# Performance work log

Hardware: AMD Instinct MI355X
Metric: run time of the kernel (lower is better)

The kernel has to match this reference:

```python
import jax, jax.numpy as jnp
import numpy as np

N = 50000       # nodes (src == dst set for both blocks)
E = 800000      # edges (avg degree 16)
IN_DIM = 64     # input node feature dim ('attr')
POT_DIM = 16    # potential feature dim ('pot')
H = 64          # h_dim == out_dim == out_edim


def setup_inputs() -> dict:
    key = jax.random.key(0)
    ks = jax.random.split(key, 14)
    g = lambda k, shape, scale: jax.random.normal(k, shape, dtype=jnp.float32) * scale
    return {
        'attr':    g(ks[0], (N, IN_DIM), 1.0),
        'pot0':    g(ks[1], (N, POT_DIM), 1.0),
        'pot1':    g(ks[2], (N, POT_DIM), 1.0),
        'edge_t0': g(ks[3], (E, H), 1.0),
        'edge_t1': g(ks[4], (E, H), 1.0),
        # pot_encoder: Linear(pot_dim, h_dim) + Tanh
        'Wpot': g(ks[5], (POT_DIM, H), POT_DIM ** -0.5),
        'bpot': jnp.zeros((H,), jnp.float32),
        # layer 0: GATLayer(in_dim, h, h, h)
        'fcW0': g(ks[6], (IN_DIM, H), IN_DIM ** -0.5),
        'fcU0': g(ks[7], (IN_DIM, H), IN_DIM ** -0.5),
        'a0':   g(ks[8], (3 * H,), (3 * H) ** -0.5),   # attn_fc weight [z_src|z_dst|t]
        'gate0': jnp.ones((H,), jnp.float32),
        # layer 1: GATLayer(h, h, h, h)
        'fcW1': g(ks[9], (H, H), H ** -0.5),
        'fcU1': g(ks[10], (H, H), H ** -0.5),
        'a1':   g(ks[11], (3 * H,), (3 * H) ** -0.5),
        'gate1': jnp.ones((H,), jnp.float32),
        'src_idx': jax.random.randint(ks[12], (E,), 0, N),
        'dst_idx': jax.random.randint(ks[13], (E,), 0, N),
    }


def _gat_layer(h, v_i, t, src, dst, fcW, fcU, a, gate):
    # h: [N, Din], v_i: [N, H], t: [E, H] (raw edge data 'd'->'t' per original forward)
    Hd = fcW.shape[1]
    z = h @ fcW                 # [N, H] srcdata['z']
    z_i = h @ fcU               # [N, H] dstdata['z_i'] (src set == dst set)
    a_src, a_dst, a_t = a[:Hd], a[Hd:2 * Hd], a[2 * Hd:]
    # attn_fc(cat[z_src, z_dst, t]) decomposed into per-node + per-edge dot products
    score = jax.nn.leaky_relu((z @ a_src)[src] + (z @ a_dst)[dst] + t @ a_t,
                              negative_slope=0.01)        # [E]
    # edge softmax over each dst node's incoming edges
    m = jax.ops.segment_max(score, dst, num_segments=N)   # [N]
    ex = jnp.exp(score - m[dst])                          # [E]
    denom = jax.ops.segment_sum(ex, dst, num_segments=N)  # [N]
    alpha = ex / jnp.where(denom == 0, 1.0, denom)[dst]   # [E]
    z_neighbor = jax.ops.segment_sum(alpha[:, None] * z[src], dst, num_segments=N)
    return z_neighbor + gate * v_i * z_i                  # [N, H]


def reference(attr, pot0, pot1, edge_t0, edge_t1, Wpot, bpot,
              fcW0, fcU0, a0, gate0, fcW1, fcU1, a1, gate1,
              src_idx, dst_idx):
    v0 = jnp.tanh(pot0 @ Wpot + bpot)
    h = _gat_layer(attr, v0, edge_t0, src_idx, dst_idx, fcW0, fcU0, a0, gate0)
    v1 = jnp.tanh(pot1 @ Wpot + bpot)
    h = _gat_layer(h, v1, edge_t1, src_idx, dst_idx, fcW1, fcU1, a1, gate1)
    return h
```

## Files before the change

### kernel.cpp

```cpp
#include <hip/hip_runtime.h>
#include <math.h>

#define NN 50000
#define EE 800000
#define BM 64
#define HB 3125
#define DB 1250
#define DS_ (DB * 256)
#define TB 782

typedef float f4 __attribute__((ext_vector_type(4)));


#define FMA4(acc, s, v) do { \
    (acc).x = fmaf((s), (v).x, (acc).x); \
    (acc).y = fmaf((s), (v).y, (acc).y); \
    (acc).z = fmaf((s), (v).z, (acc).z); \
    (acc).w = fmaf((s), (v).w, (acc).w); } while (0)

__device__ __forceinline__ float dot4(float4 u, float4 v) {
    return fmaf(u.x, v.x, fmaf(u.y, v.y, fmaf(u.z, v.z, u.w * v.w)));
}

__device__ __forceinline__ unsigned pk_bf16(float lo, float hi) {
    union { float f; unsigned u; } a, b;
    a.f = lo; b.f = hi;
    unsigned alo = (a.u + 0x7FFFu + ((a.u >> 16) & 1u)) >> 16;
    unsigned bhi = (b.u + 0x7FFFu + ((b.u >> 16) & 1u)) >> 16;
    return (bhi << 16) | alo;
}

__device__ __forceinline__ float upk_bf16(unsigned u, int odd) {
    union { unsigned u; float f; } r;
    r.u = odd ? (u & 0xFFFF0000u) : (u << 16);
    return r.f;
}


__global__ __launch_bounds__(256) void hist_dot(
    const int* __restrict__ dst, int* __restrict__ deg, int* __restrict__ rank,
    const float* __restrict__ et0, const float* __restrict__ et1,
    const float* __restrict__ a0, const float* __restrict__ a1,
    float* __restrict__ sc0, float* __restrict__ sc1)
{
    const int bid = blockIdx.x;

    if (bid < HB) {
        const int e = bid * 256 + threadIdx.x;
        rank[e] = atomicAdd(&deg[dst[e]], 1);
    } else {
        const int tid  = (bid - HB) * 256 + threadIdx.x;
        const int lane = threadIdx.x & 63;
        const int p    = tid & 15;
        const float4 A0 = *reinterpret_cast<const float4*>(a0 + 128 + p * 4);
        const float4 A1 = *reinterpret_cast<const float4*>(a1 + 128 + p * 4);
        const f4* __restrict__ e0 = reinterpret_cast<const f4*>(et0);
        const f4* __restrict__ e1 = reinterpret_cast<const f4*>(et1);

        for (int i = tid; i < EE * 16; i += DS_ * 8) {
            f4 v0[8], v1[8];
#pragma unroll
            for (int u = 0; u < 8; u++) v0[u] = __builtin_nontemporal_load(e0 + i + u * DS_);
#pragma unroll
            for (int u = 0; u < 8; u++) v1[u] = __builtin_nontemporal_load(e1 + i + u * DS_);
            float r0[8], r1[8];
#pragma unroll
            for (int u = 0; u < 8; u++) {
                r0[u] = fmaf(v0[u][0], A0.x, fmaf(v0[u][1], A0.y, fmaf(v0[u][2], A0.z, v0[u][3] * A0.w)));
                r1[u] = fmaf(v1[u][0], A1.x, fmaf(v1[u][1], A1.y, fmaf(v1[u][2], A1.z, v1[u][3] * A1.w)));
            }
#pragma unroll
            for (int u = 0; u < 8; u++) {
#pragma unroll
                for (int off = 8; off; off >>= 1) {
                    r0[u] += __shfl_xor(r0[u], off);
                    r1[u] += __shfl_xor(r1[u], off);
                }
            }
            if ((lane & 15) == 0) {
#pragma unroll
                for (int u = 0; u < 8; u++) {
                    const int e = (i + u * DS_) >> 4;
                    sc0[e] = r0[u];
                    sc1[e] = r1[u];
                }
            }
        }
    }
}


__global__ __launch_bounds__(1024) void k_scan(int* __restrict__ deg, int* __restrict__ rowptr) {
    __shared__ int part[1024];
    const int t  = threadIdx.x;
    const int CH = (NN + 1023) / 1024;
    const int b  = t * CH;
    const int e  = min(b + CH, NN);
    int sum = 0;
    for (int i = b; i < e; i++) sum += deg[i];
    part[t] = sum;
    __syncthreads();
    for (int off = 1; off < 1024; off <<= 1) {
        int v = (t >= off) ? part[t - off] : 0;
        __syncthreads();
        part[t] += v;
        __syncthreads();
    }
    int run = (t == 0) ? 0 : part[t - 1];
    for (int i = b; i < e; i++) {
        rowptr[i] = run;
        run += deg[i];
    }
    if (t == 0) rowptr[NN] = EE;
}

__global__ __launch_bounds__(256) void k_scatter(const int* __restrict__ src, const int* __restrict__ dst,
                                                 const int* __restrict__ rowptr, const int* __restrict__ rank,
                                                 int2* __restrict__ epair) {
    int e = blockIdx.x * 256 + threadIdx.x;
    if (e < EE) {
        int p = rowptr[dst[e]] + rank[e];
        epair[p] = make_int2(e, src[e]);
    }
}


__global__ __launch_bounds__(256) void node_transform(
    const float* __restrict__ hin, const float* __restrict__ pot,
    const float* __restrict__ Wpot, const float* __restrict__ bpot,
    const float* __restrict__ fcW, const float* __restrict__ fcU,
    const float* __restrict__ a, const float* __restrict__ gate,
    unsigned* __restrict__ zb, float* __restrict__ zs, float* __restrict__ zd,
    float* __restrict__ base)
{
    __shared__ float sAt[64][64];
    __shared__ float sB[64][128];
    __shared__ float sPot[64][16];
    __shared__ float sWp[16][64];

    const int t     = threadIdx.x;
    const int m0    = blockIdx.x * BM;
    const int valid = min(BM, NN - m0);

#pragma unroll
    for (int j = 0; j < 4; j++) {
        const int idx = t + j * 256;
        const int kw = idx >> 4, cq = idx & 15;
        *reinterpret_cast<float4*>(&sB[kw][cq * 4]) =
            *reinterpret_cast<const float4*>(fcW + kw * 64 + cq * 4);
        *reinterpret_cast<float4*>(&sB[kw][64 + cq * 4]) =
            *reinterpret_cast<const float4*>(fcU + kw * 64 + cq * 4);
    }
    {
        const int m = t >> 2, q = t & 3;
#pragma unroll
        for (int i = 0; i < 4; i++) {
            const int kg = i * 4 + q;
            float4 v4 = make_float4(0.f, 0.f, 0.f, 0.f);
            if (m < valid)
                v4 = *reinterpret_cast<const float4*>(hin + (size_t)(m0 + m) * 64 + kg * 4);
            sAt[kg * 4 + 0][m] = v4.x;
            sAt[kg * 4 + 1][m] = v4.y;
            sAt[kg * 4 + 2][m] = v4.z;
            sAt[kg * 4 + 3][m] = v4.w;
        }
        float4 p4 = make_float4(0.f, 0.f, 0.f, 0.f);
        if (m < valid)
            p4 = *reinterpret_cast<const float4*>(pot + (size_t)(m0 + m) * 16 + q * 4);
        *reinterpret_cast<float4*>(&sPot[m][q * 4]) = p4;
    }
    {
        const int kk = t >> 4, cq = t & 15;
        *reinterpret_cast<float4*>(&sWp[kk][cq * 4]) =
            *reinterpret_cast<const float4*>(Wpot + kk * 64 + cq * 4);
    }
    __syncthreads();

    const int c4 = (t & 15) * 4;
    const int r4 = (t >> 4) * 4;

    float4 az[4], au[4];
#pragma unroll
    for (int i = 0; i < 4; i++) {
        az[i] = make_float4(0.f, 0.f, 0.f, 0.f);
        au[i] = make_float4(0.f, 0.f, 0.f, 0.f);
    }

#pragma unroll 4
    for (int k = 0; k < 64; k++) {
        const float4 a4 = *reinterpret_cast<const float4*>(&sAt[k][r4]);
        const float4 bw = *reinterpret_cast<const float4*>(&sB[k][c4]);
        const float4 bu = *reinterpret_cast<const float4*>(&sB[k][64 + c4]);
        FMA4(az[0], a4.x, bw); FMA4(au[0], a4.x, bu);
        FMA4(az[1], a4.y, bw); FMA4(au[1], a4.y, bu);
        FMA4(az[2], a4.z, bw); FMA4(au[2], a4.z, bu);
        FMA4(az[3], a4.w, bw); FMA4(au[3], a4.w, bu);
    }

    {
        const float4 as4 = *reinterpret_cast<const float4*>(a + c4);
        const float4 ad4 = *reinterpret_cast<const float4*>(a + 64 + c4);
        float ps[4], pd[4];
#pragma unroll
        for (int i = 0; i < 4; i++) { ps[i] = dot4(az[i], as4); pd[i] = dot4(az[i], ad4); }
#pragma unroll
        for (int off = 1; off < 16; off <<= 1) {
#pragma unroll
            for (int i = 0; i < 4; i++) {
                ps[i] += __shfl_xor(ps[i], off);
                pd[i] += __shfl_xor(pd[i], off);
            }
        }
        if ((t & 15) == 0) {
#pragma unroll
            for (int i = 0; i < 4; i++) {
                if (r4 + i < valid) {
                    zs[m0 + r4 + i] = ps[i];
                    zd[m0 + r4 + i] = pd[i];
                }
            }
        }
    }

    {
        const float4 bp4 = *reinterpret_cast<const float4*>(bpot + c4);
        const float4 g4  = *reinterpret_cast<const float4*>(gate + c4);
        float4 vv[4] = {bp4, bp4, bp4, bp4};
#pragma unroll
        for (int kk = 0; kk < 16; kk++) {
            const float4 wp = *reinterpret_cast<const float4*>(&sWp[kk][c4]);
#pragma unroll
            for (int i = 0; i < 4; i++) {
                const float pv = sPot[r4 + i][kk];
                FMA4(vv[i], pv, wp);
            }
        }
#pragma unroll
        for (int i = 0; i < 4; i++) {
            if (r4 + i < valid) {
                const int n = m0 + r4 + i;
                uint2 zp;
                zp.x = pk_bf16(az[i].x, az[i].y);
                zp.y = pk_bf16(az[i].z, az[i].w);
                *reinterpret_cast<uint2*>(zb + (size_t)n * 32 + c4 / 2) = zp;
                float4 b;
                b.x = g4.x * tanhf(vv[i].x) * au[i].x;
                b.y = g4.y * tanhf(vv[i].y) * au[i].y;
                b.z = g4.z * tanhf(vv[i].z) * au[i].z;
                b.w = g4.w * tanhf(vv[i].w) * au[i].w;
                *reinterpret_cast<float4*>(base + (size_t)n * 64 + c4) = b;
            }
        }
    }
}


__global__ __launch_bounds__(256) void node_sm_agg(
    const int* __restrict__ rowptr, const int2* __restrict__ epair,
    const float* __restrict__ score_t, const float* __restrict__ zs, const float* __restrict__ zd,
    const unsigned* __restrict__ zb, const float* __restrict__ base,
    float* __restrict__ out)
{
    const int lane = threadIdx.x & 63;
    const int n    = blockIdx.x * 4 + (threadIdx.x >> 6);
    if (n >= NN) return;

    const int s0  = rowptr[n], s1 = rowptr[n + 1];
    const int deg = s1 - s0;
    const float zdn = zd[n];
    const int half = lane >> 1;
    const int odd  = lane & 1;

    float acc = 0.f;
    float ds;

    if (deg <= 64) {
        const int j = s0 + lane;
        int   sv = 0;
        float sc = -INFINITY;
        if (j < s1) {
            const int2 pr = epair[j];
            sv = pr.y;
            float v = score_t[pr.x] + zs[sv] + zdn;
            sc = (v >= 0.f) ? v : 0.01f * v;
        }
        float mx = sc;
#pragma unroll
        for (int off = 32; off; off >>= 1) mx = fmaxf(mx, __shfl_xor(mx, off));
        float ex = (j < s1) ? __expf(sc - mx) : 0.f;
        ds = ex;
#pragma unroll
        for (int off = 32; off; off >>= 1) ds += __shfl_xor(ds, off);

        int t = 0;
        for (; t + 8 <= deg; t += 8) {
            int   ss[8]; float ee[8]; unsigned uu[8];
#pragma unroll
            for (int u = 0; u < 8; u++) {
                ss[u] = __shfl(sv, t + u);
                ee[u] = __shfl(ex, t + u);
            }
#pragma unroll
            for (int u = 0; u < 8; u++) uu[u] = zb[(size_t)ss[u] * 32 + half];
#pragma unroll
            for (int u = 0; u < 8; u++) acc = fmaf(ee[u], upk_bf16(uu[u], odd), acc);
        }
        for (; t + 4 <= deg; t += 4) {
            int   ss[4]; float ee[4]; unsigned uu[4];
#pragma unroll
            for (int u = 0; u < 4; u++) {
                ss[u] = __shfl(sv, t + u);
                ee[u] = __shfl(ex, t + u);
            }
#pragma unroll
            for (int u = 0; u < 4; u++) uu[u] = zb[(size_t)ss[u] * 32 + half];
#pragma unroll
            for (int u = 0; u < 4; u++) acc = fmaf(ee[u], upk_bf16(uu[u], odd), acc);
        }
        for (; t < deg; t++) {
            int   s = __shfl(sv, t);
            float e = __shfl(ex, t);
            acc = fmaf(e, upk_bf16(zb[(size_t)s * 32 + half], odd), acc);
        }
    } else {
        float mx = -INFINITY;
        for (int j = s0 + lane; j < s1; j += 64) {
            const int2 pr = epair[j];
            float v = score_t[pr.x] + zs[pr.y] + zdn;
            v = (v >= 0.f) ? v : 0.01f * v;
            mx = fmaxf(mx, v);
        }
#pragma unroll
        for (int off = 32; off; off >>= 1) mx = fmaxf(mx, __shfl_xor(mx, off));
        ds = 0.f;
        for (int c0 = s0; c0 < s1; c0 += 64) {
            const int j = c0 + lane;
            int   sv = 0;
            float ex = 0.f;
            if (j < s1) {
                const int2 pr = epair[j];
                sv = pr.y;
                float v = score_t[pr.x] + zs[sv] + zdn;
                v = (v >= 0.f) ? v : 0.01f * v;
                ex = __expf(v - mx);
            }
            ds += ex;
            const int cnt = min(64, s1 - c0);
            for (int t = 0; t < cnt; t++) {
                int   s = __shfl(sv, t);
                float e = __shfl(ex, t);
                acc = fmaf(e, upk_bf16(zb[(size_t)s * 32 + half], odd), acc);
            }
        }
#pragma unroll
        for (int off = 32; off; off >>= 1) ds += __shfl_xor(ds, off);
    }

    float r = 1.f / ((ds == 0.f) ? 1.f : ds);
    const size_t o = (size_t)n * 64 + lane;
    out[o] = acc * r + base[o];
}


extern "C" void kernel_launch(void* const* d_in, const int* in_sizes, int n_in,
                              void* d_out, int out_size, void* d_ws, size_t ws_size,
                              hipStream_t stream)
{
    const float* attr  = (const float*)d_in[0];
    const float* pot0  = (const float*)d_in[1];
    const float* pot1  = (const float*)d_in[2];
    const float* et0   = (const float*)d_in[3];
    const float* et1   = (const float*)d_in[4];
    const float* Wpot  = (const float*)d_in[5];
    const float* bpot  = (const float*)d_in[6];
    const float* fcW0  = (const float*)d_in[7];
    const float* fcU0  = (const float*)d_in[8];
    const float* a0    = (const float*)d_in[9];
    const float* gate0 = (const float*)d_in[10];
    const float* fcW1  = (const float*)d_in[11];
    const float* fcU1  = (const float*)d_in[12];
    const float* a1    = (const float*)d_in[13];
    const float* gate1 = (const float*)d_in[14];
    const int*   src   = (const int*)d_in[15];
    const int*   dst   = (const int*)d_in[16];

    float* out = (float*)d_out;

    float*    ws     = (float*)d_ws;
    unsigned* zb     = (unsigned*)ws;
    float*    base   = (float*)(zb + NN * 32);
    float*    zs     = base + NN * 64;
    float*    zd     = zs + NN;
    float*    sc0    = zd + NN;
    float*    sc1    = sc0 + EE;
    int*      rowptr = (int*)(sc1 + EE);
    int*      deg    = rowptr + NN + 2;
    int*      rank   = deg + NN;
    int2*     epair  = (int2*)(rank + EE);

    const int eblk = (EE + 255) / 256;
    const int nblk = (NN + 3) / 4;

    hipMemsetAsync(deg, 0, NN * sizeof(int), stream);

    hist_dot<<<HB + DB, 256, 0, stream>>>(dst, deg, rank, et0, et1, a0, a1, sc0, sc1);

    node_transform<<<TB, 256, 0, stream>>>(attr, pot0, Wpot, bpot, fcW0, fcU0,
                                           a0, gate0, zb, zs, zd, base);

    k_scan<<<1, 1024, 0, stream>>>(deg, rowptr);
    k_scatter<<<eblk, 256, 0, stream>>>(src, dst, rowptr, rank, epair);

    node_sm_agg<<<nblk, 256, 0, stream>>>(rowptr, epair, sc0, zs, zd, zb, base, out);

    node_transform<<<TB, 256, 0, stream>>>(out, pot1, Wpot, bpot, fcW1, fcU1,
                                           a1, gate1, zb, zs, zd, base);
    node_sm_agg<<<nblk, 256, 0, stream>>>(rowptr, epair, sc1, zs, zd, zb, base, out);
}
```

Before: 337.8 us.

## Pack edge scores into CSR edge pairs and fold scan into node transform

The scatter kernel now writes per-layer (src, score) pairs in CSR order, so the aggregation kernel reads the edge score contiguously instead of gathering score_t by original edge id. The prefix scan moves from its own single-block launch into an extra block of the first node_transform launch, removing one kernel launch. The edge-dot loop doubles its block count and halves its unroll. The scatter now writes twice as much data, and the scan now runs with 256 threads instead of 1024.

After: 330.7 us. 1.02x faster.

```diff
diff --git a/kernel.cpp b/kernel.cpp
--- a/kernel.cpp
+++ b/kernel.cpp
@@ -5,8 +5,8 @@
 #define EE 800000
 #define BM 64
 #define HB 3125
-#define DB 1250
-#define DS_ (DB * 256)
+#define DB 2500
+#define DS2 (DB * 256)
 #define TB 782
 
 typedef float f4 __attribute__((ext_vector_type(4)));
@@ -57,20 +57,20 @@
         const f4* __restrict__ e0 = reinterpret_cast<const f4*>(et0);
         const f4* __restrict__ e1 = reinterpret_cast<const f4*>(et1);
 
-        for (int i = tid; i < EE * 16; i += DS_ * 8) {
-            f4 v0[8], v1[8];
-#pragma unroll
-            for (int u = 0; u < 8; u++) v0[u] = __builtin_nontemporal_load(e0 + i + u * DS_);
-#pragma unroll
-            for (int u = 0; u < 8; u++) v1[u] = __builtin_nontemporal_load(e1 + i + u * DS_);
-            float r0[8], r1[8];
-#pragma unroll
-            for (int u = 0; u < 8; u++) {
+        for (int i = tid; i < EE * 16; i += DS2 * 4) {
+            f4 v0[4], v1[4];
+#pragma unroll
+            for (int u = 0; u < 4; u++) v0[u] = __builtin_nontemporal_load(e0 + i + u * DS2);
+#pragma unroll
+            for (int u = 0; u < 4; u++) v1[u] = __builtin_nontemporal_load(e1 + i + u * DS2);
+            float r0[4], r1[4];
+#pragma unroll
+            for (int u = 0; u < 4; u++) {
                 r0[u] = fmaf(v0[u][0], A0.x, fmaf(v0[u][1], A0.y, fmaf(v0[u][2], A0.z, v0[u][3] * A0.w)));
                 r1[u] = fmaf(v1[u][0], A1.x, fmaf(v1[u][1], A1.y, fmaf(v1[u][2], A1.z, v1[u][3] * A1.w)));
             }
 #pragma unroll
-            for (int u = 0; u < 8; u++) {
+            for (int u = 0; u < 4; u++) {
 #pragma unroll
                 for (int off = 8; off; off >>= 1) {
                     r0[u] += __shfl_xor(r0[u], off);
@@ -79,8 +79,8 @@
             }
             if ((lane & 15) == 0) {
 #pragma unroll
-                for (int u = 0; u < 8; u++) {
-                    const int e = (i + u * DS_) >> 4;
+                for (int u = 0; u < 4; u++) {
+                    const int e = (i + u * DS2) >> 4;
                     sc0[e] = r0[u];
                     sc1[e] = r1[u];
                 }
@@ -90,37 +90,18 @@
 }
 
 
-__global__ __launch_bounds__(1024) void k_scan(int* __restrict__ deg, int* __restrict__ rowptr) {
-    __shared__ int part[1024];
-    const int t  = threadIdx.x;
-    const int CH = (NN + 1023) / 1024;
-    const int b  = t * CH;
-    const int e  = min(b + CH, NN);
-    int sum = 0;
-    for (int i = b; i < e; i++) sum += deg[i];
-    part[t] = sum;
-    __syncthreads();
-    for (int off = 1; off < 1024; off <<= 1) {
-        int v = (t >= off) ? part[t - off] : 0;
-        __syncthreads();
-        part[t] += v;
-        __syncthreads();
-    }
-    int run = (t == 0) ? 0 : part[t - 1];
-    for (int i = b; i < e; i++) {
-        rowptr[i] = run;
-        run += deg[i];
-    }
-    if (t == 0) rowptr[NN] = EE;
-}
-
-__global__ __launch_bounds__(256) void k_scatter(const int* __restrict__ src, const int* __restrict__ dst,
-                                                 const int* __restrict__ rowptr, const int* __restrict__ rank,
-                                                 int2* __restrict__ epair) {
+__global__ __launch_bounds__(256) void k_scatter(
+    const int* __restrict__ src, const int* __restrict__ dst,
+    const int* __restrict__ rowptr, const int* __restrict__ rank,
+    const float* __restrict__ sc0, const float* __restrict__ sc1,
+    int2* __restrict__ epA, int2* __restrict__ epB)
+{
     int e = blockIdx.x * 256 + threadIdx.x;
     if (e < EE) {
-        int p = rowptr[dst[e]] + rank[e];
-        epair[p] = make_int2(e, src[e]);
+        const int p = rowptr[dst[e]] + rank[e];
+        const int s = src[e];
+        epA[p] = make_int2(s, __float_as_int(sc0[e]));
+        epB[p] = make_int2(s, __float_as_int(sc1[e]));
     }
 }
 
@@ -131,14 +112,40 @@
     const float* __restrict__ fcW, const float* __restrict__ fcU,
     const float* __restrict__ a, const float* __restrict__ gate,
     unsigned* __restrict__ zb, float* __restrict__ zs, float* __restrict__ zd,
-    float* __restrict__ base)
+    float* __restrict__ base,
+    const int* __restrict__ deg, int* __restrict__ rowptr, int do_scan)
 {
     __shared__ float sAt[64][64];
     __shared__ float sB[64][128];
     __shared__ float sPot[64][16];
     __shared__ float sWp[16][64];
 
-    const int t     = threadIdx.x;
+    const int t = threadIdx.x;
+
+    if (do_scan && blockIdx.x == TB) {
+        int* part = reinterpret_cast<int*>(&sAt[0][0]);
+        const int CH = (NN + 255) / 256;
+        const int b  = t * CH;
+        const int e  = min(b + CH, NN);
+        int sum = 0;
+        for (int i = b; i < e; i++) sum += deg[i];
+        part[t] = sum;
+        __syncthreads();
+        for (int off = 1; off < 256; off <<= 1) {
+            int v = (t >= off) ? part[t - off] : 0;
+            __syncthreads();
+            part[t] += v;
+            __syncthreads();
+        }
+        int run = (t == 0) ? 0 : part[t - 1];
+        for (int i = b; i < e; i++) {
+            rowptr[i] = run;
+            run += deg[i];
+        }
+        if (t == 0) rowptr[NN] = EE;
+        return;
+    }
+
     const int m0    = blockIdx.x * BM;
     const int valid = min(BM, NN - m0);
 
@@ -256,8 +263,8 @@
 
 
 __global__ __launch_bounds__(256) void node_sm_agg(
-    const int* __restrict__ rowptr, const int2* __restrict__ epair,
-    const float* __restrict__ score_t, const float* __restrict__ zs, const float* __restrict__ zd,
+    const int* __restrict__ rowptr, const int2* __restrict__ ep,
+    const float* __restrict__ zs, const float* __restrict__ zd,
     const unsigned* __restrict__ zb, const float* __restrict__ base,
     float* __restrict__ out)
 {
@@ -279,9 +286,9 @@
         int   sv = 0;
         float sc = -INFINITY;
         if (j < s1) {
-            const int2 pr = epair[j];
-            sv = pr.y;
-            float v = score_t[pr.x] + zs[sv] + zdn;
+            const int2 pr = ep[j];
+            sv = pr.x;
+            float v = __int_as_float(pr.y) + zs[sv] + zdn;
             sc = (v >= 0.f) ? v : 0.01f * v;
         }
         float mx = sc;
@@ -325,8 +332,8 @@
     } else {
         float mx = -INFINITY;
         for (int j = s0 + lane; j < s1; j += 64) {
-            const int2 pr = epair[j];
-            float v = score_t[pr.x] + zs[pr.y] + zdn;
+            const int2 pr = ep[j];
+            float v = __int_as_float(pr.y) + zs[pr.x] + zdn;
             v = (v >= 0.f) ? v : 0.01f * v;
             mx = fmaxf(mx, v);
         }
@@ -338,9 +345,9 @@
             int   sv = 0;
             float ex = 0.f;
             if (j < s1) {
-                const int2 pr = epair[j];
-                sv = pr.y;
-                float v = score_t[pr.x] + zs[sv] + zdn;
+                const int2 pr = ep[j];
+                sv = pr.x;
+                float v = __int_as_float(pr.y) + zs[sv] + zdn;
                 v = (v >= 0.f) ? v : 0.01f * v;
                 ex = __expf(v - mx);
             }
@@ -386,17 +393,17 @@
 
     float* out = (float*)d_out;
 
-    float*    ws     = (float*)d_ws;
-    unsigned* zb     = (unsigned*)ws;
+    int2*     epA    = (int2*)d_ws;
+    int2*     epB    = epA + EE;
+    unsigned* zb     = (unsigned*)(epB + EE);
     float*    base   = (float*)(zb + NN * 32);
     float*    zs     = base + NN * 64;
     float*    zd     = zs + NN;
     float*    sc0    = zd + NN;
     float*    sc1    = sc0 + EE;
     int*      rowptr = (int*)(sc1 + EE);
-    int*      deg    = rowptr + NN + 2;
+    int*      deg    = rowptr + NN + 1;
     int*      rank   = deg + NN;
-    int2*     epair  = (int2*)(rank + EE);
 
     const int eblk = (EE + 255) / 256;
     const int nblk = (NN + 3) / 4;
@@ -405,15 +412,16 @@
 
     hist_dot<<<HB + DB, 256, 0, stream>>>(dst, deg, rank, et0, et1, a0, a1, sc0, sc1);
 
-    node_transform<<<TB, 256, 0, stream>>>(attr, pot0, Wpot, bpot, fcW0, fcU0,
-                                           a0, gate0, zb, zs, zd, base);
-
-    k_scan<<<1, 1024, 0, stream>>>(deg, rowptr);
-    k_scatter<<<eblk, 256, 0, stream>>>(src, dst, rowptr, rank, epair);
-
-    node_sm_agg<<<nblk, 256, 0, stream>>>(rowptr, epair, sc0, zs, zd, zb, base, out);
+    node_transform<<<TB + 1, 256, 0, stream>>>(attr, pot0, Wpot, bpot, fcW0, fcU0,
+                                               a0, gate0, zb, zs, zd, base,
+                                               deg, rowptr, 1);
+
+    k_scatter<<<eblk, 256, 0, stream>>>(src, dst, rowptr, rank, sc0, sc1, epA, epB);
+
+    node_sm_agg<<<nblk, 256, 0, stream>>>(rowptr, epA, zs, zd, zb, base, out);
 
     node_transform<<<TB, 256, 0, stream>>>(out, pot1, Wpot, bpot, fcW1, fcU1,
-                                           a1, gate1, zb, zs, zd, base);
-    node_sm_agg<<<nblk, 256, 0, stream>>>(rowptr, epair, sc1, zs, zd, zb, base, out);
-}
+                                           a1, gate1, zb, zs, zd, base,
+                                           deg, rowptr, 0);
+    node_sm_agg<<<nblk, 256, 0, stream>>>(rowptr, epB, zs, zd, zb, base, out);
+}
```
